# Kernel optimization log

Measured on AMD Instinct MI355X. Metric: run time of the kernel, lower is better.

The kernel has to match this reference:

```python
import jax, jax.numpy as jnp
import numpy as np

K = 3            # kernel size
PAD = 1          # padding for kernel_size=3
EPS = 1e-5       # BatchNorm eps
B, C, H, W = 8, 64, 256, 256


def deform_conv2d(x, offset, weight):
    """torchvision-style deform_conv2d, stride=1, pad=1, 1 offset group, no bias.
    x: [B, Cin, H, W]; offset: [B, 2*K*K, H, W] interleaved (dy, dx) per tap;
    weight: [Cout, Cin, K, K]."""
    b, cin, h, w = x.shape
    k2 = K * K
    off = offset.reshape(b, k2, 2, h, w)
    dy, dx = off[:, :, 0], off[:, :, 1]                 # [B,K2,H,W]
    kh = jnp.repeat(jnp.arange(K), K).astype(x.dtype)   # tap row, torch order k=kh*K+kw
    kw = jnp.tile(jnp.arange(K), K).astype(x.dtype)     # tap col
    # sampling positions: out pixel (i,j), tap k -> (i - PAD + kh + dy, j - PAD + kw + dx)
    py = dy + (jnp.arange(h, dtype=x.dtype) - PAD)[None, None, :, None] + kh[None, :, None, None]
    px = dx + (jnp.arange(w, dtype=x.dtype) - PAD)[None, None, None, :] + kw[None, :, None, None]

    y0 = jnp.floor(py); x0 = jnp.floor(px)
    wy = py - y0; wx = px - x0                          # bilinear fractions
    iy0 = y0.astype(jnp.int32); ix0 = x0.astype(jnp.int32)
    iy1 = iy0 + 1; ix1 = ix0 + 1

    xf = x.reshape(b, cin, h * w)

    def gather(iy, ix):
        valid = ((iy >= 0) & (iy < h) & (ix >= 0) & (ix < w)).astype(x.dtype)
        idx = jnp.clip(iy, 0, h - 1) * w + jnp.clip(ix, 0, w - 1)   # [B,K2,H,W]
        v = jax.vmap(lambda xi, ii: xi[:, ii])(xf, idx.reshape(b, -1))  # [B,Cin,K2*H*W]
        return v.reshape(b, cin, k2, h, w) * valid[:, None]

    sampled = ((1 - wy) * (1 - wx))[:, None] * gather(iy0, ix0) \
            + ((1 - wy) * wx)[:, None]       * gather(iy0, ix1) \
            + (wy * (1 - wx))[:, None]       * gather(iy1, ix0) \
            + (wy * wx)[:, None]             * gather(iy1, ix1)   # [B,Cin,K2,H,W]

    wk = weight.reshape(weight.shape[0], cin, k2)
    return jnp.einsum('bckhw,ock->bohw', sampled, wk)


def setup_inputs() -> dict:
    key = jax.random.key(0)
    k1, k2, k3 = jax.random.split(key, 3)
    x = jax.random.normal(k1, (B, C, H, W), dtype=jnp.float32)
    offset = jax.random.normal(k2, (B, 2 * K * K, H, W), dtype=jnp.float32)
    weight = jax.random.normal(k3, (1, 2, K, K), dtype=jnp.float32) * 0.1  # Conv2d(2,1,3)
    gamma = jnp.ones((1,), dtype=jnp.float32)
    beta = jnp.zeros((1,), dtype=jnp.float32)
    return {"x": x, "offset": offset, "weight": weight, "gamma": gamma, "beta": beta}


def reference(x, offset, weight, gamma, beta):
    avg_out = jnp.mean(x, axis=1, keepdims=True)
    max_out = jnp.max(x, axis=1, keepdims=True)
    feat = jnp.concatenate([avg_out, max_out], axis=1)      # [B,2,H,W]
    out = deform_conv2d(feat, offset, weight)               # [B,1,H,W]
    # BatchNorm2d (training-mode batch statistics)
    mu = jnp.mean(out, axis=(0, 2, 3), keepdims=True)
    var = jnp.var(out, axis=(0, 2, 3), keepdims=True)
    out = gamma.reshape(1, -1, 1, 1) * (out - mu) * jax.lax.rsqrt(var + EPS) + beta.reshape(1, -1, 1, 1)
    return x * jax.nn.sigmoid(out)
```

## Files before the change

kernel.cpp:

```cpp
#include <hip/hip_runtime.h>
#include <math.h>

#define BB 8
#define CC 64
#define HH 256
#define WW 256
#define HWp (HH * WW)
#define BHW (BB * HWp)
#define NK 9

__global__ __launch_bounds__(256) void reduce_c_kernel(
    const float* __restrict__ x, float* __restrict__ favg, float* __restrict__ fmax) {
    int t = blockIdx.x * 256 + threadIdx.x;
    int b = t / (HWp / 4);
    int p = t - b * (HWp / 4);
    const float4* xp = reinterpret_cast<const float4*>(x) + (size_t)b * CC * (HWp / 4) + p;
    float4 s = make_float4(0.f, 0.f, 0.f, 0.f);
    float4 m = make_float4(-INFINITY, -INFINITY, -INFINITY, -INFINITY);
#pragma unroll 16
    for (int c = 0; c < CC; ++c) {
        float4 v = xp[(size_t)c * (HWp / 4)];
        s.x += v.x; s.y += v.y; s.z += v.z; s.w += v.w;
        m.x = fmaxf(m.x, v.x); m.y = fmaxf(m.y, v.y);
        m.z = fmaxf(m.z, v.z); m.w = fmaxf(m.w, v.w);
    }
    const float inv = 1.0f / CC;
    reinterpret_cast<float4*>(favg)[t] = make_float4(s.x * inv, s.y * inv, s.z * inv, s.w * inv);
    reinterpret_cast<float4*>(fmax)[t] = m;
}

__device__ __forceinline__ float2 bisample(const float* __restrict__ fa,
                                           const float* __restrict__ fm,
                                           int iy, int ix) {
    bool v = ((unsigned)iy < (unsigned)HH) && ((unsigned)ix < (unsigned)WW);
    int cy = iy < 0 ? 0 : (iy > HH - 1 ? HH - 1 : iy);
    int cx = ix < 0 ? 0 : (ix > WW - 1 ? WW - 1 : ix);
    int idx = cy * WW + cx;
    float a = v ? fa[idx] : 0.f;
    float m = v ? fm[idx] : 0.f;
    return make_float2(a, m);
}

__global__ __launch_bounds__(256) void dconv_kernel(
    const float* __restrict__ off, const float* __restrict__ wgt,
    const float* __restrict__ favg, const float* __restrict__ fmax,
    float* __restrict__ outmap, float* __restrict__ accum) {
    int t = blockIdx.x * 256 + threadIdx.x;
    int b = t >> 16;
    int p = t & (HWp - 1);
    int h = p >> 8;
    int w = p & (WW - 1);

    const float* ob = off + (size_t)b * (2 * NK) * HWp + p;
    const float* fa = favg + b * HWp;
    const float* fm = fmax + b * HWp;

    float wk[2 * NK];
#pragma unroll
    for (int i = 0; i < 2 * NK; ++i) wk[i] = wgt[i];

    float acc = 0.f;
#pragma unroll
    for (int k = 0; k < NK; ++k) {
        float dy = ob[(size_t)(2 * k) * HWp];
        float dx = ob[(size_t)(2 * k + 1) * HWp];
        float py = dy + (float)(h - 1 + k / 3);
        float px = dx + (float)(w - 1 + k % 3);
        float y0 = floorf(py), x0 = floorf(px);
        float wy = py - y0, wx = px - x0;
        int iy0 = (int)y0, ix0 = (int)x0;
        float w00 = (1.f - wy) * (1.f - wx);
        float w01 = (1.f - wy) * wx;
        float w10 = wy * (1.f - wx);
        float w11 = wy * wx;
        float2 c00 = bisample(fa, fm, iy0, ix0);
        float2 c01 = bisample(fa, fm, iy0, ix0 + 1);
        float2 c10 = bisample(fa, fm, iy0 + 1, ix0);
        float2 c11 = bisample(fa, fm, iy0 + 1, ix0 + 1);
        float s0 = w00 * c00.x + w01 * c01.x + w10 * c10.x + w11 * c11.x;
        float s1 = w00 * c00.y + w01 * c01.y + w10 * c10.y + w11 * c11.y;
        acc += wk[k] * s0 + wk[NK + k] * s1;
    }
    outmap[t] = acc;

    float s1r = acc, s2r = acc * acc;
#pragma unroll
    for (int o = 32; o > 0; o >>= 1) {
        s1r += __shfl_down(s1r, o, 64);
        s2r += __shfl_down(s2r, o, 64);
    }
    __shared__ float ls1[4], ls2[4];
    int lane = threadIdx.x & 63, wid = threadIdx.x >> 6;
    if (lane == 0) { ls1[wid] = s1r; ls2[wid] = s2r; }
    __syncthreads();
    if (threadIdx.x == 0) {
        float t1 = ls1[0] + ls1[1] + ls1[2] + ls1[3];
        float t2 = ls2[0] + ls2[1] + ls2[2] + ls2[3];
        atomicAdd(&accum[0], t1);
        atomicAdd(&accum[1], t2);
    }
}

__global__ __launch_bounds__(256) void sig_kernel(
    const float* __restrict__ outmap, const float* __restrict__ accum,
    const float* __restrict__ gamma, const float* __restrict__ beta,
    float* __restrict__ sigmap) {
    int t = blockIdx.x * 256 + threadIdx.x;
    float mu = accum[0] * (1.0f / BHW);
    float var = accum[1] * (1.0f / BHW) - mu * mu;
    float rs = rsqrtf(var + 1e-5f);
    float g = gamma[0], be = beta[0];
    float4 o = reinterpret_cast<const float4*>(outmap)[t];
    float4 r;
    r.x = 1.f / (1.f + expf(-(g * (o.x - mu) * rs + be)));
    r.y = 1.f / (1.f + expf(-(g * (o.y - mu) * rs + be)));
    r.z = 1.f / (1.f + expf(-(g * (o.z - mu) * rs + be)));
    r.w = 1.f / (1.f + expf(-(g * (o.w - mu) * rs + be)));
    reinterpret_cast<float4*>(sigmap)[t] = r;
}

__global__ __launch_bounds__(256) void final_kernel(
    const float* __restrict__ x, const float* __restrict__ sigmap,
    float* __restrict__ out) {
    size_t t = (size_t)blockIdx.x * 256 + threadIdx.x;
    const int per_b = CC * (HWp / 4);
    int b = (int)(t / per_b);
    int rem = (int)(t - (size_t)b * per_b);
    int p4 = rem & (HWp / 4 - 1);
    float4 xv = reinterpret_cast<const float4*>(x)[t];
    float4 sv = reinterpret_cast<const float4*>(sigmap)[b * (HWp / 4) + p4];
    reinterpret_cast<float4*>(out)[t] =
        make_float4(xv.x * sv.x, xv.y * sv.y, xv.z * sv.z, xv.w * sv.w);
}

extern "C" void kernel_launch(void* const* d_in, const int* in_sizes, int n_in,
                              void* d_out, int out_size, void* d_ws, size_t ws_size,
                              hipStream_t stream) {
    const float* x      = (const float*)d_in[0];
    const float* offset = (const float*)d_in[1];
    const float* weight = (const float*)d_in[2];
    const float* gamma  = (const float*)d_in[3];
    const float* beta   = (const float*)d_in[4];
    float* out = (float*)d_out;

    float* ws     = (float*)d_ws;
    float* favg   = ws;
    float* fmax   = ws + BHW;
    float* outmap = ws + 2 * BHW;
    float* accum  = ws + 3 * BHW;
    float* sigmap = favg;

    hipMemsetAsync(accum, 0, 2 * sizeof(float), stream);

    reduce_c_kernel<<<(BHW / 4) / 256, 256, 0, stream>>>(x, favg, fmax);
    dconv_kernel<<<BHW / 256, 256, 0, stream>>>(offset, weight, favg, fmax, outmap, accum);
    sig_kernel<<<(BHW / 4) / 256, 256, 0, stream>>>(outmap, accum, gamma, beta, sigmap);
    final_kernel<<<((size_t)BB * CC * HWp / 4) / 256, 256, 0, stream>>>(x, sigmap, out);
}
```

Baseline: 341.5 us.

## Interleave avg/max features into float2 layout, use nontemporal stores, drop memset

The channel-reduced avg and max maps are now stored interleaved as float2, so each bilinear tap in the deformable conv needs one 8-byte gather instead of two separate 4-byte gathers. Stores of the feature map and of the final output use nontemporal hints to limit cache pollution. The separate memset of the BN accumulators is replaced by zeroing them inside the first kernel. Vector ext types replace float4 for simpler arithmetic. The nontemporal feature store may evict data the dconv kernel reads soon after.

```diff
diff --git a/kernel.cpp b/kernel.cpp
--- a/kernel.cpp
+++ b/kernel.cpp
@@ -9,42 +9,44 @@
 #define BHW (BB * HWp)
 #define NK 9
 
+typedef float f32x4 __attribute__((ext_vector_type(4)));
+
 __global__ __launch_bounds__(256) void reduce_c_kernel(
-    const float* __restrict__ x, float* __restrict__ favg, float* __restrict__ fmax) {
+    const float* __restrict__ x, float* __restrict__ feat, float* __restrict__ accum) {
     int t = blockIdx.x * 256 + threadIdx.x;
+    if (blockIdx.x == 0 && threadIdx.x < 2) accum[threadIdx.x] = 0.f;
     int b = t / (HWp / 4);
     int p = t - b * (HWp / 4);
-    const float4* xp = reinterpret_cast<const float4*>(x) + (size_t)b * CC * (HWp / 4) + p;
-    float4 s = make_float4(0.f, 0.f, 0.f, 0.f);
-    float4 m = make_float4(-INFINITY, -INFINITY, -INFINITY, -INFINITY);
+    const f32x4* xp = reinterpret_cast<const f32x4*>(x) + (size_t)b * CC * (HWp / 4) + p;
+    f32x4 s = {0.f, 0.f, 0.f, 0.f};
+    f32x4 m = {-INFINITY, -INFINITY, -INFINITY, -INFINITY};
 #pragma unroll 16
     for (int c = 0; c < CC; ++c) {
-        float4 v = xp[(size_t)c * (HWp / 4)];
-        s.x += v.x; s.y += v.y; s.z += v.z; s.w += v.w;
+        f32x4 v = xp[(size_t)c * (HWp / 4)];
+        s += v;
         m.x = fmaxf(m.x, v.x); m.y = fmaxf(m.y, v.y);
         m.z = fmaxf(m.z, v.z); m.w = fmaxf(m.w, v.w);
     }
     const float inv = 1.0f / CC;
-    reinterpret_cast<float4*>(favg)[t] = make_float4(s.x * inv, s.y * inv, s.z * inv, s.w * inv);
-    reinterpret_cast<float4*>(fmax)[t] = m;
+    f32x4 o0 = {s.x * inv, m.x, s.y * inv, m.y};
+    f32x4 o1 = {s.z * inv, m.z, s.w * inv, m.w};
+    f32x4* fp = reinterpret_cast<f32x4*>(feat) + 2 * (size_t)t;
+    __builtin_nontemporal_store(o0, fp);
+    __builtin_nontemporal_store(o1, fp + 1);
 }
 
-__device__ __forceinline__ float2 bisample(const float* __restrict__ fa,
-                                           const float* __restrict__ fm,
-                                           int iy, int ix) {
+__device__ __forceinline__ float2 bisample(const float2* __restrict__ f, int iy, int ix) {
     bool v = ((unsigned)iy < (unsigned)HH) && ((unsigned)ix < (unsigned)WW);
     int cy = iy < 0 ? 0 : (iy > HH - 1 ? HH - 1 : iy);
     int cx = ix < 0 ? 0 : (ix > WW - 1 ? WW - 1 : ix);
-    int idx = cy * WW + cx;
-    float a = v ? fa[idx] : 0.f;
-    float m = v ? fm[idx] : 0.f;
-    return make_float2(a, m);
+    float2 r = f[cy * WW + cx];
+    return v ? r : make_float2(0.f, 0.f);
 }
 
 __global__ __launch_bounds__(256) void dconv_kernel(
     const float* __restrict__ off, const float* __restrict__ wgt,
-    const float* __restrict__ favg, const float* __restrict__ fmax,
-    float* __restrict__ outmap, float* __restrict__ accum) {
+    const float* __restrict__ feat, float* __restrict__ outmap,
+    float* __restrict__ accum) {
     int t = blockIdx.x * 256 + threadIdx.x;
     int b = t >> 16;
     int p = t & (HWp - 1);
@@ -52,8 +54,7 @@
     int w = p & (WW - 1);
 
     const float* ob = off + (size_t)b * (2 * NK) * HWp + p;
-    const float* fa = favg + b * HWp;
-    const float* fm = fmax + b * HWp;
+    const float2* f = reinterpret_cast<const float2*>(feat) + (size_t)b * HWp;
 
     float wk[2 * NK];
 #pragma unroll
@@ -73,10 +74,10 @@
         float w01 = (1.f - wy) * wx;
         float w10 = wy * (1.f - wx);
         float w11 = wy * wx;
-        float2 c00 = bisample(fa, fm, iy0, ix0);
-        float2 c01 = bisample(fa, fm, iy0, ix0 + 1);
-        float2 c10 = bisample(fa, fm, iy0 + 1, ix0);
-        float2 c11 = bisample(fa, fm, iy0 + 1, ix0 + 1);
+        float2 c00 = bisample(f, iy0, ix0);
+        float2 c01 = bisample(f, iy0, ix0 + 1);
+        float2 c10 = bisample(f, iy0 + 1, ix0);
+        float2 c11 = bisample(f, iy0 + 1, ix0 + 1);
         float s0 = w00 * c00.x + w01 * c01.x + w10 * c10.x + w11 * c11.x;
         float s1 = w00 * c00.y + w01 * c01.y + w10 * c10.y + w11 * c11.y;
         acc += wk[k] * s0 + wk[NK + k] * s1;
@@ -110,13 +111,13 @@
     float var = accum[1] * (1.0f / BHW) - mu * mu;
     float rs = rsqrtf(var + 1e-5f);
     float g = gamma[0], be = beta[0];
-    float4 o = reinterpret_cast<const float4*>(outmap)[t];
-    float4 r;
+    f32x4 o = reinterpret_cast<const f32x4*>(outmap)[t];
+    f32x4 r;
     r.x = 1.f / (1.f + expf(-(g * (o.x - mu) * rs + be)));
     r.y = 1.f / (1.f + expf(-(g * (o.y - mu) * rs + be)));
     r.z = 1.f / (1.f + expf(-(g * (o.z - mu) * rs + be)));
     r.w = 1.f / (1.f + expf(-(g * (o.w - mu) * rs + be)));
-    reinterpret_cast<float4*>(sigmap)[t] = r;
+    reinterpret_cast<f32x4*>(sigmap)[t] = r;
 }
 
 __global__ __launch_bounds__(256) void final_kernel(
@@ -127,10 +128,10 @@
     int b = (int)(t / per_b);
     int rem = (int)(t - (size_t)b * per_b);
     int p4 = rem & (HWp / 4 - 1);
-    float4 xv = reinterpret_cast<const float4*>(x)[t];
-    float4 sv = reinterpret_cast<const float4*>(sigmap)[b * (HWp / 4) + p4];
-    reinterpret_cast<float4*>(out)[t] =
-        make_float4(xv.x * sv.x, xv.y * sv.y, xv.z * sv.z, xv.w * sv.w);
+    f32x4 xv = reinterpret_cast<const f32x4*>(x)[t];
+    f32x4 sv = reinterpret_cast<const f32x4*>(sigmap)[b * (HWp / 4) + p4];
+    f32x4 r = xv * sv;
+    __builtin_nontemporal_store(r, reinterpret_cast<f32x4*>(out) + t);
 }
 
 extern "C" void kernel_launch(void* const* d_in, const int* in_sizes, int n_in,
@@ -144,16 +145,13 @@
     float* out = (float*)d_out;
 
     float* ws     = (float*)d_ws;
-    float* favg   = ws;
-    float* fmax   = ws + BHW;
+    float* feat   = ws;
     float* outmap = ws + 2 * BHW;
     float* accum  = ws + 3 * BHW;
-    float* sigmap = favg;
+    float* sigmap = feat;
 
-    hipMemsetAsync(accum, 0, 2 * sizeof(float), stream);
-
-    reduce_c_kernel<<<(BHW / 4) / 256, 256, 0, stream>>>(x, favg, fmax);
-    dconv_kernel<<<BHW / 256, 256, 0, stream>>>(offset, weight, favg, fmax, outmap, accum);
+    reduce_c_kernel<<<(BHW / 4) / 256, 256, 0, stream>>>(x, feat, accum);
+    dconv_kernel<<<BHW / 256, 256, 0, stream>>>(offset, weight, feat, outmap, accum);
     sig_kernel<<<(BHW / 4) / 256, 256, 0, stream>>>(outmap, accum, gamma, beta, sigmap);
     final_kernel<<<((size_t)BB * CC * HWp / 4) / 256, 256, 0, stream>>>(x, sigmap, out);
 }
```

Measured after the change: 334.0 us. 2.2% less time.
